# Optimization experiments

Measured on AMD Instinct MI355X. Metric: run time of the kernel, lower is better.

The kernel has to match this reference:

```python
import jax, jax.numpy as jnp
import numpy as np

B = 128        # graphs in batch
GW = 30        # grid width (nodes per graph = GW*GW)
IW = 90        # image width = 3*GW for k=7,s=3,p=2 conv transpose
C_IN = 32
HID = [64, 64, 32]
R = 8          # num relations
NB = 4         # num bases
N = B * GW * GW          # 115200 nodes
E = N * 8                # 921600 edges
NEG_SLOPE = 0.01         # F.leaky_relu default


def setup_inputs() -> dict:
    key = jax.random.key(0)
    ks = jax.random.split(key, 24)
    inp = {
        "features": jax.random.normal(ks[0], (N, C_IN), jnp.float32),
        "src": jax.random.randint(ks[1], (E,), 0, N),
        "dst": jax.random.randint(ks[2], (E,), 0, N),
        "etypes": jax.random.randint(ks[3], (E,), 0, R),
        "norm": jax.random.uniform(ks[4], (E,), jnp.float32),
    }
    dims = [C_IN] + HID
    for l in range(3):
        din, dout = dims[l], dims[l + 1]
        s = 1.0 / np.sqrt(din)
        inp[f"bases{l}"] = jax.random.normal(ks[5 + 4 * l], (NB, din, dout), jnp.float32) * s
        inp[f"comp{l}"] = jax.random.normal(ks[6 + 4 * l], (R, NB), jnp.float32) * (1.0 / np.sqrt(NB))
        inp[f"loop{l}"] = jax.random.normal(ks[7 + 4 * l], (din, dout), jnp.float32) * s
        inp[f"bias{l}"] = jnp.zeros((dout,), jnp.float32)
    inp["conv_w"] = jax.random.normal(ks[20], (HID[-1], 1, 7, 7), jnp.float32) * 0.05  # torch ConvT layout (Cin,Cout,kH,kW)
    inp["conv_b"] = jnp.zeros((1,), jnp.float32)
    return inp


def _rel_graph_conv(h, bases, comp, loop_w, bias, src, dst, etypes, norm, act):
    # basis decomposition: W_r = sum_b comp[r,b] * bases[b]   -> (R, in, out)
    W = jnp.einsum("rb,bio->rio", comp, bases)
    # project every node by every relation weight, then gather per edge
    proj = jnp.einsum("ni,rio->nro", h, W)          # (N, R, out)
    msg = proj[src, etypes] * norm[:, None]          # (E, out)
    agg = jax.ops.segment_sum(msg, dst, num_segments=h.shape[0])
    out = agg + h @ loop_w + bias                    # self-loop + bias (DGL defaults)
    return act(out)


def _conv_transpose(x, w_torch, b, stride, pad):
    # torch ConvTranspose2d(w: (Cin,Cout,kH,kW)) == dilated conv with flipped kernel
    k = w_torch.shape[-1]
    w = jnp.flip(w_torch, (2, 3)).transpose(1, 0, 2, 3)  # -> OIHW
    p = k - 1 - pad
    y = jax.lax.conv_general_dilated(
        x, w, window_strides=(1, 1), padding=[(p, p), (p, p)],
        lhs_dilation=(stride, stride),
        dimension_numbers=("NCHW", "OIHW", "NCHW"))
    return y + b[None, :, None, None]


def reference(features, src, dst, etypes, norm,
              bases0, comp0, loop0, bias0,
              bases1, comp1, loop1, bias1,
              bases2, comp2, loop2, bias2,
              conv_w, conv_b):
    leaky = lambda x: jnp.where(x >= 0, x, NEG_SLOPE * x)
    h = _rel_graph_conv(features, bases0, comp0, loop0, bias0, src, dst, etypes, norm, leaky)
    h = _rel_graph_conv(h, bases1, comp1, loop1, bias1, src, dst, etypes, norm, leaky)
    logits = _rel_graph_conv(h, bases2, comp2, loop2, bias2, src, dst, etypes, norm, jax.nn.sigmoid)
    # every graph has exactly GW*GW nodes -> vectorized decode (replaces per-graph loop)
    x = logits.reshape(B, GW, GW, HID[-1]).transpose(0, 3, 1, 2)  # (B, C, GW, GW)
    y = jax.nn.sigmoid(_conv_transpose(x, conv_w, conv_b, stride=3, pad=2))  # (B,1,IW,IW)
    return y.reshape(B, IW, IW)
```

## Files before the change

kernel.cpp:

```cpp
#include <hip/hip_runtime.h>
#include <hip/hip_bf16.h>

#define B_GR   128
#define GWID   30
#define IWID   90
#define C_IN   32
#define R_REL  8
#define NBAS   4
#define N_NODES (B_GR*GWID*GWID)
#define E_EDGES (N_NODES*8)
#define NEG_SLOPE 0.01f

#define SCAN_BLOCKS (N_NODES/256)

typedef __attribute__((ext_vector_type(8))) __bf16 bf16x8;
typedef __attribute__((ext_vector_type(4))) float f32x4;

__global__ void k_bases_t(const float* __restrict__ bases, __bf16* __restrict__ Bt,
                          int din, int dout) {
    int idx = blockIdx.x*256 + threadIdx.x;
    int tot = NBAS*din*dout;
    if (idx >= tot) return;
    int b = idx/(dout*din), rem = idx%(dout*din);
    int c = rem/din, k = rem%din;
    Bt[idx] = (__bf16)bases[((size_t)b*din + k)*dout + c];
}
__global__ void k_loop_t(const float* __restrict__ loopw, __bf16* __restrict__ loopt,
                         int din, int dout) {
    int idx = blockIdx.x*256 + threadIdx.x;
    if (idx >= din*dout) return;
    int c = idx/din, k = idx%din;
    loopt[idx] = (__bf16)loopw[(size_t)k*dout + c];
}

__global__ void k_deg(const int* __restrict__ dst, int* __restrict__ deg) {
    int e = blockIdx.x*256 + threadIdx.x;
    if (e < E_EDGES) atomicAdd(&deg[dst[e]], 1);
}
__global__ __launch_bounds__(256) void k_scan1(const int* __restrict__ deg,
                                               int* __restrict__ rowptr,
                                               int* __restrict__ bsum) {
    __shared__ int s[256], s2[256];
    const int tid = threadIdx.x, gid = blockIdx.x*256 + tid;
    int v = deg[gid];
    s[tid] = v;
    __syncthreads();
    int* cur = s; int* nxt = s2;
    for (int d = 1; d < 256; d <<= 1) {
        int val = cur[tid];
        if (tid >= d) val += cur[tid - d];
        nxt[tid] = val;
        __syncthreads();
        int* t = cur; cur = nxt; nxt = t;
    }
    rowptr[gid] = cur[tid] - v;
    if (tid == 255) bsum[blockIdx.x] = cur[255];
}
__global__ __launch_bounds__(512) void k_scan2(int* __restrict__ bsum, int* __restrict__ rowptr) {
    __shared__ int s[512], s2[512];
    const int tid = threadIdx.x;
    int v = (tid < SCAN_BLOCKS) ? bsum[tid] : 0;
    s[tid] = v;
    __syncthreads();
    int* cur = s; int* nxt = s2;
    for (int d = 1; d < 512; d <<= 1) {
        int val = cur[tid];
        if (tid >= d) val += cur[tid - d];
        nxt[tid] = val;
        __syncthreads();
        int* t = cur; cur = nxt; nxt = t;
    }
    if (tid < SCAN_BLOCKS) bsum[tid] = cur[tid] - v;
    if (tid == 0) rowptr[N_NODES] = E_EDGES;
}
__global__ void k_scan3(int* __restrict__ rowptr, const int* __restrict__ bsum,
                        int* __restrict__ cursor) {
    int gid = blockIdx.x*256 + threadIdx.x;
    int v = rowptr[gid] + bsum[blockIdx.x];
    rowptr[gid] = v;
    cursor[gid] = v;
}
__global__ void k_scatter_pack(const int* __restrict__ src, const int* __restrict__ dst,
                               const int* __restrict__ et, const float* __restrict__ norm,
                               int* __restrict__ cursor, int2* __restrict__ pmeta) {
    int e = blockIdx.x*256 + threadIdx.x;
    if (e < E_EDGES) {
        int pos = atomicAdd(&cursor[dst[e]], 1);
        int2 m;
        m.x = src[e] | (et[e] << 24);
        m.y = __float_as_int(norm[e]);
        pmeta[pos] = m;
    }
}

template<int DIN, int DOUT, int ACT, int IN_F32, int OUT_F32, int MINW>
__global__ __launch_bounds__(256, MINW) void k_fusedb(
        const void* __restrict__ hin, const __bf16* __restrict__ Bt,
        const __bf16* __restrict__ loopt, const float* __restrict__ bias,
        const float* __restrict__ comp, const int* __restrict__ rowptr,
        const int2* __restrict__ pmeta, void* __restrict__ hout) {
    constexpr int KS = DIN/32;
    constexpr int NF = DOUT/16;
    const int tid = threadIdx.x;
    const int w = tid >> 6, l = tid & 63;
    const int m = l & 15, g = l >> 4;
    const int nb = blockIdx.x*64 + w*16;
    const int node = nb + m;

    f32x4 acc[NF];
    #pragma unroll
    for (int nf = 0; nf < NF; ++nf) acc[nf] = (f32x4){0.f,0.f,0.f,0.f};

    float ka[NBAS][KS][8];
    #pragma unroll
    for (int b = 0; b < NBAS; ++b)
        #pragma unroll
        for (int ks = 0; ks < KS; ++ks)
            #pragma unroll
            for (int c = 0; c < 8; ++c) ka[b][ks][c] = 0.f;

    const int jb = rowptr[node], je = rowptr[node+1];
    int2 mt = pmeta[jb];
    for (int j = jb; j < je; ++j) {
        const int2 mtn = pmeta[j+1];
        const int p = mt.x & 0xFFFFFF;
        const int et = ((unsigned)mt.x) >> 24;
        const float nm = __int_as_float(mt.y);
        const float4 cw = *(const float4*)(comp + et*NBAS);
        const float w0 = nm*cw.x, w1 = nm*cw.y, w2 = nm*cw.z, w3 = nm*cw.w;
        float hv[KS][8];
        if (IN_F32) {
            const float* hp = (const float*)hin + (size_t)p*DIN + g*8;
            #pragma unroll
            for (int ks = 0; ks < KS; ++ks) {
                float4 v0 = *(const float4*)(hp + ks*32);
                float4 v1 = *(const float4*)(hp + ks*32 + 4);
                hv[ks][0]=v0.x; hv[ks][1]=v0.y; hv[ks][2]=v0.z; hv[ks][3]=v0.w;
                hv[ks][4]=v1.x; hv[ks][5]=v1.y; hv[ks][6]=v1.z; hv[ks][7]=v1.w;
            }
        } else {
            const __bf16* hp = (const __bf16*)hin + (size_t)p*DIN + g*8;
            #pragma unroll
            for (int ks = 0; ks < KS; ++ks) {
                bf16x8 v = *(const bf16x8*)(hp + ks*32);
                #pragma unroll
                for (int c = 0; c < 8; ++c) hv[ks][c] = (float)v[c];
            }
        }
        #pragma unroll
        for (int ks = 0; ks < KS; ++ks) {
            #pragma unroll
            for (int c = 0; c < 8; ++c) {
                ka[0][ks][c] += w0*hv[ks][c];
                ka[1][ks][c] += w1*hv[ks][c];
                ka[2][ks][c] += w2*hv[ks][c];
                ka[3][ks][c] += w3*hv[ks][c];
            }
        }
        mt = mtn;
    }

    #pragma unroll
    for (int b = 0; b < NBAS; ++b) {
        #pragma unroll
        for (int ks = 0; ks < KS; ++ks) {
            bf16x8 fa;
            #pragma unroll
            for (int c = 0; c < 8; ++c) fa[c] = (__bf16)ka[b][ks][c];
            #pragma unroll
            for (int nf = 0; nf < NF; ++nf) {
                bf16x8 fb = *(const bf16x8*)(Bt + ((size_t)b*DOUT + nf*16 + m)*DIN
                                             + ks*32 + g*8);
                acc[nf] = __builtin_amdgcn_mfma_f32_16x16x32_bf16(fa, fb, acc[nf], 0, 0, 0);
            }
        }
    }

    #pragma unroll
    for (int ks = 0; ks < KS; ++ks) {
        bf16x8 fa;
        if (IN_F32) {
            const float* hp = (const float*)hin + (size_t)node*DIN + ks*32 + g*8;
            float4 v0 = *(const float4*)hp;
            float4 v1 = *(const float4*)(hp + 4);
            fa[0]=(__bf16)v0.x; fa[1]=(__bf16)v0.y; fa[2]=(__bf16)v0.z; fa[3]=(__bf16)v0.w;
            fa[4]=(__bf16)v1.x; fa[5]=(__bf16)v1.y; fa[6]=(__bf16)v1.z; fa[7]=(__bf16)v1.w;
        } else {
            fa = *(const bf16x8*)((const __bf16*)hin + (size_t)node*DIN + ks*32 + g*8);
        }
        #pragma unroll
        for (int nf = 0; nf < NF; ++nf) {
            bf16x8 fb = *(const bf16x8*)(loopt + (size_t)(nf*16 + m)*DIN + ks*32 + g*8);
            acc[nf] = __builtin_amdgcn_mfma_f32_16x16x32_bf16(fa, fb, acc[nf], 0, 0, 0);
        }
    }

    #pragma unroll
    for (int nf = 0; nf < NF; ++nf) {
        const int col = nf*16 + m;
        const float bv = bias[col];
        #pragma unroll
        for (int ri = 0; ri < 4; ++ri) {
            const int orow = nb + g*4 + ri;
            float v = acc[nf][ri] + bv;
            if (ACT == 0) v = (v >= 0.f) ? v : NEG_SLOPE*v;
            else          v = 1.f/(1.f + __expf(-v));
            if (OUT_F32) ((float*)hout)[(size_t)orow*DOUT + col] = v;
            else         ((__bf16*)hout)[(size_t)orow*DOUT + col] = (__bf16)v;
        }
    }
}

__global__ __launch_bounds__(256) void k_convt_f32(const float* __restrict__ logits,
        const float* __restrict__ w, const float* __restrict__ cb, float* __restrict__ out) {
    __shared__ float s_w[49*32];
    const int tid = threadIdx.x;
    for (int idx = tid; idx < 49*32; idx += 256) {
        int tap = idx/32, c = idx%32;
        s_w[tap*32 + c] = w[c*49 + tap];
    }
    __syncthreads();
    int gidx = blockIdx.x*256 + tid;
    if (gidx >= B_GR*IWID*IWID) return;
    int b = gidx/(IWID*IWID);
    int rem = gidx%(IWID*IWID);
    int oy = rem/IWID, ox = rem%IWID;

    const int py = (oy+2)%3, qy = (oy+2)/3;
    const int px = (ox+2)%3, qx = (ox+2)/3;

    float acc = cb[0];
    #pragma unroll
    for (int sy = 0; sy < 3; ++sy) {
        const int ky = py + 3*sy;
        const int iy = qy - sy;
        if (ky > 6 || iy < 0 || iy >= GWID) continue;
        #pragma unroll
        for (int sx = 0; sx < 3; ++sx) {
            const int kx = px + 3*sx;
            const int ix = qx - sx;
            if (kx > 6 || ix < 0 || ix >= GWID) continue;
            const float4* xp = (const float4*)&logits[(((size_t)b*GWID + iy)*GWID + ix)*32];
            const float4* wp = (const float4*)&s_w[(ky*7 + kx)*32];
            #pragma unroll
            for (int c4 = 0; c4 < 8; ++c4) {
                float4 xv = xp[c4], wv = wp[c4];
                acc += xv.x*wv.x + xv.y*wv.y + xv.z*wv.z + xv.w*wv.w;
            }
        }
    }
    out[gidx] = 1.f/(1.f + __expf(-acc));
}

extern "C" void kernel_launch(void* const* d_in, const int* in_sizes, int n_in,
                              void* d_out, int out_size, void* d_ws, size_t ws_size,
                              hipStream_t stream) {
    const float* features = (const float*)d_in[0];
    const int*   src      = (const int*)  d_in[1];
    const int*   dst      = (const int*)  d_in[2];
    const int*   etypes   = (const int*)  d_in[3];
    const float* norm     = (const float*)d_in[4];
    const float* bases0 = (const float*)d_in[5];
    const float* comp0  = (const float*)d_in[6];
    const float* loop0  = (const float*)d_in[7];
    const float* bias0  = (const float*)d_in[8];
    const float* bases1 = (const float*)d_in[9];
    const float* comp1  = (const float*)d_in[10];
    const float* loop1  = (const float*)d_in[11];
    const float* bias1  = (const float*)d_in[12];
    const float* bases2 = (const float*)d_in[13];
    const float* comp2  = (const float*)d_in[14];
    const float* loop2  = (const float*)d_in[15];
    const float* bias2  = (const float*)d_in[16];
    const float* conv_w = (const float*)d_in[17];
    const float* conv_b = (const float*)d_in[18];
    float* out = (float*)d_out;

    const int ebl = (E_EDGES + 255)/256;
    float* ws = (float*)d_ws;
    auto pad4 = [](size_t v){ return (v + 3) & ~(size_t)3; };

    size_t off = 0;
    __bf16* Bt0   = (__bf16*)(ws + off); off += (size_t)NBAS*32*64/2;
    __bf16* Bt1   = (__bf16*)(ws + off); off += (size_t)NBAS*64*64/2;
    __bf16* Bt2   = (__bf16*)(ws + off); off += (size_t)NBAS*64*32/2;
    __bf16* lt0   = (__bf16*)(ws + off); off += (size_t)64*32/2;
    __bf16* lt1   = (__bf16*)(ws + off); off += (size_t)64*64/2;
    __bf16* lt2   = (__bf16*)(ws + off); off += (size_t)32*64/2;
    __bf16* h1    = (__bf16*)(ws + off); off += (size_t)N_NODES*64/2;
    __bf16* h2    = (__bf16*)(ws + off); off += (size_t)N_NODES*64/2;
    float*  lg    = (float*)(ws + off);  off += (size_t)N_NODES*32;
    int* rowptr   = (int*)(ws + off); off += pad4((size_t)N_NODES + 4);
    int* deg      = (int*)(ws + off); off += (size_t)N_NODES;
    int* bsum     = (int*)(ws + off); off += 512;
    int2* pmeta   = (int2*)(ws + off); off += (size_t)(E_EDGES + 4)*2;

    k_bases_t<<<(NBAS*32*64 + 255)/256, 256, 0, stream>>>(bases0, Bt0, 32, 64);
    k_bases_t<<<(NBAS*64*64 + 255)/256, 256, 0, stream>>>(bases1, Bt1, 64, 64);
    k_bases_t<<<(NBAS*64*32 + 255)/256, 256, 0, stream>>>(bases2, Bt2, 64, 32);
    k_loop_t<<<(32*64 + 255)/256, 256, 0, stream>>>(loop0, lt0, 32, 64);
    k_loop_t<<<(64*64 + 255)/256, 256, 0, stream>>>(loop1, lt1, 64, 64);
    k_loop_t<<<(64*32 + 255)/256, 256, 0, stream>>>(loop2, lt2, 64, 32);

    hipMemsetAsync(deg, 0, (size_t)N_NODES*sizeof(int), stream);
    k_deg  <<<ebl, 256, 0, stream>>>(dst, deg);
    k_scan1<<<SCAN_BLOCKS, 256, 0, stream>>>(deg, rowptr, bsum);
    k_scan2<<<1, 512, 0, stream>>>(bsum, rowptr);
    k_scan3<<<SCAN_BLOCKS, 256, 0, stream>>>(rowptr, bsum, deg);
    k_scatter_pack<<<ebl, 256, 0, stream>>>(src, dst, etypes, norm, deg, pmeta);

    const int NROWT = N_NODES/64;

    k_fusedb<32,64,0,1,0,4><<<NROWT, 256, 0, stream>>>(features, Bt0, lt0, bias0, comp0,
                                                       rowptr, pmeta, h1);
    k_fusedb<64,64,0,0,0,3><<<NROWT, 256, 0, stream>>>(h1, Bt1, lt1, bias1, comp1,
                                                       rowptr, pmeta, h2);
    k_fusedb<64,32,1,0,1,3><<<NROWT, 256, 0, stream>>>(h2, Bt2, lt2, bias2, comp2,
                                                       rowptr, pmeta, lg);

    k_convt_f32<<<(B_GR*IWID*IWID + 255)/256, 256, 0, stream>>>(lg, conv_w, conv_b, out);
}
```

Before: 337.9 us.

## Split each node's edge list across four waves and reduce partial results in LDS

Each block now covers 16 nodes instead of 64. The four waves each take a quarter of every node's incoming edges, aggregate them, and run their own basis MFMAs. Waves 1-3 write their accumulators to shared memory, and wave 0 adds them, applies the self-loop, bias and activation, then stores. This shortens the serial per-lane gather loop and adds memory-level parallelism. The cost is four times the basis MFMA work and weight loads, plus an LDS reduction and a barrier, with three waves idle during the epilogue.

```diff
diff --git a/kernel.cpp b/kernel.cpp
--- a/kernel.cpp
+++ b/kernel.cpp
@@ -94,23 +94,30 @@
 }
 
 template<int DIN, int DOUT, int ACT, int IN_F32, int OUT_F32, int MINW>
-__global__ __launch_bounds__(256, MINW) void k_fusedb(
+__global__ __launch_bounds__(256, MINW) void k_fusedb4(
         const void* __restrict__ hin, const __bf16* __restrict__ Bt,
         const __bf16* __restrict__ loopt, const float* __restrict__ bias,
         const float* __restrict__ comp, const int* __restrict__ rowptr,
         const int2* __restrict__ pmeta, void* __restrict__ hout) {
     constexpr int KS = DIN/32;
     constexpr int NF = DOUT/16;
+    __shared__ float lds_acc[3][NF*4][64];
     const int tid = threadIdx.x;
     const int w = tid >> 6, l = tid & 63;
     const int m = l & 15, g = l >> 4;
-    const int nb = blockIdx.x*64 + w*16;
-    const int node = nb + m;
+    const int node0 = blockIdx.x*16;
+    const int node = node0 + m;
 
     f32x4 acc[NF];
     #pragma unroll
     for (int nf = 0; nf < NF; ++nf) acc[nf] = (f32x4){0.f,0.f,0.f,0.f};
 
+    const int jb = rowptr[node], je = rowptr[node+1];
+    const int len = je - jb;
+    const int q = (len + 3) >> 2;
+    const int wb = jb + w*q;
+    const int we = (wb + q < je) ? (wb + q) : je;
+
     float ka[NBAS][KS][8];
     #pragma unroll
     for (int b = 0; b < NBAS; ++b)
@@ -119,45 +126,46 @@
             #pragma unroll
             for (int c = 0; c < 8; ++c) ka[b][ks][c] = 0.f;
 
-    const int jb = rowptr[node], je = rowptr[node+1];
-    int2 mt = pmeta[jb];
-    for (int j = jb; j < je; ++j) {
-        const int2 mtn = pmeta[j+1];
-        const int p = mt.x & 0xFFFFFF;
-        const int et = ((unsigned)mt.x) >> 24;
-        const float nm = __int_as_float(mt.y);
-        const float4 cw = *(const float4*)(comp + et*NBAS);
-        const float w0 = nm*cw.x, w1 = nm*cw.y, w2 = nm*cw.z, w3 = nm*cw.w;
-        float hv[KS][8];
-        if (IN_F32) {
-            const float* hp = (const float*)hin + (size_t)p*DIN + g*8;
+    if (wb < we) {
+        int2 mt = pmeta[wb];
+        for (int j = wb; j < we; ++j) {
+            const int2 mtn = pmeta[j+1];
+            const int p = mt.x & 0xFFFFFF;
+            const int et = ((unsigned)mt.x) >> 24;
+            const float nm = __int_as_float(mt.y);
+            const float4 cw = *(const float4*)(comp + et*NBAS);
+            const float w0 = nm*cw.x, w1 = nm*cw.y, w2 = nm*cw.z, w3 = nm*cw.w;
+            float hv[KS][8];
+            if (IN_F32) {
+                const float* hp = (const float*)hin + (size_t)p*DIN + g*8;
+                #pragma unroll
+                for (int ks = 0; ks < KS; ++ks) {
+                    float4 v0 = *(const float4*)(hp + ks*32);
+                    float4 v1 = *(const float4*)(hp + ks*32 + 4);
+                    hv[ks][0]=v0.x; hv[ks][1]=v0.y; hv[ks][2]=v0.z; hv[ks][3]=v0.w;
+                    hv[ks][4]=v1.x; hv[ks][5]=v1.y; hv[ks][6]=v1.z; hv[ks][7]=v1.w;
+                }
+            } else {
+                const __bf16* hp = (const __bf16*)hin + (size_t)p*DIN + g*8;
+                #pragma unroll
+                for (int ks = 0; ks < KS; ++ks) {
+                    bf16x8 v = *(const bf16x8*)(hp + ks*32);
+                    #pragma unroll
+                    for (int c = 0; c < 8; ++c) hv[ks][c] = (float)v[c];
+                }
+            }
             #pragma unroll
             for (int ks = 0; ks < KS; ++ks) {
-                float4 v0 = *(const float4*)(hp + ks*32);
-                float4 v1 = *(const float4*)(hp + ks*32 + 4);
-                hv[ks][0]=v0.x; hv[ks][1]=v0.y; hv[ks][2]=v0.z; hv[ks][3]=v0.w;
-                hv[ks][4]=v1.x; hv[ks][5]=v1.y; hv[ks][6]=v1.z; hv[ks][7]=v1.w;
-            }
-        } else {
-            const __bf16* hp = (const __bf16*)hin + (size_t)p*DIN + g*8;
-            #pragma unroll
-            for (int ks = 0; ks < KS; ++ks) {
-                bf16x8 v = *(const bf16x8*)(hp + ks*32);
                 #pragma unroll
-                for (int c = 0; c < 8; ++c) hv[ks][c] = (float)v[c];
-            }
-        }
-        #pragma unroll
-        for (int ks = 0; ks < KS; ++ks) {
-            #pragma unroll
-            for (int c = 0; c < 8; ++c) {
-                ka[0][ks][c] += w0*hv[ks][c];
-                ka[1][ks][c] += w1*hv[ks][c];
-                ka[2][ks][c] += w2*hv[ks][c];
-                ka[3][ks][c] += w3*hv[ks][c];
-            }
-        }
-        mt = mtn;
+                for (int c = 0; c < 8; ++c) {
+                    ka[0][ks][c] += w0*hv[ks][c];
+                    ka[1][ks][c] += w1*hv[ks][c];
+                    ka[2][ks][c] += w2*hv[ks][c];
+                    ka[3][ks][c] += w3*hv[ks][c];
+                }
+            }
+            mt = mtn;
+        }
     }
 
     #pragma unroll
@@ -176,37 +184,52 @@
         }
     }
 
-    #pragma unroll
-    for (int ks = 0; ks < KS; ++ks) {
-        bf16x8 fa;
-        if (IN_F32) {
-            const float* hp = (const float*)hin + (size_t)node*DIN + ks*32 + g*8;
-            float4 v0 = *(const float4*)hp;
-            float4 v1 = *(const float4*)(hp + 4);
-            fa[0]=(__bf16)v0.x; fa[1]=(__bf16)v0.y; fa[2]=(__bf16)v0.z; fa[3]=(__bf16)v0.w;
-            fa[4]=(__bf16)v1.x; fa[5]=(__bf16)v1.y; fa[6]=(__bf16)v1.z; fa[7]=(__bf16)v1.w;
-        } else {
-            fa = *(const bf16x8*)((const __bf16*)hin + (size_t)node*DIN + ks*32 + g*8);
-        }
+    if (w == 0) {
+        #pragma unroll
+        for (int ks = 0; ks < KS; ++ks) {
+            bf16x8 fa;
+            if (IN_F32) {
+                const float* hp = (const float*)hin + (size_t)node*DIN + ks*32 + g*8;
+                float4 v0 = *(const float4*)hp;
+                float4 v1 = *(const float4*)(hp + 4);
+                fa[0]=(__bf16)v0.x; fa[1]=(__bf16)v0.y; fa[2]=(__bf16)v0.z; fa[3]=(__bf16)v0.w;
+                fa[4]=(__bf16)v1.x; fa[5]=(__bf16)v1.y; fa[6]=(__bf16)v1.z; fa[7]=(__bf16)v1.w;
+            } else {
+                fa = *(const bf16x8*)((const __bf16*)hin + (size_t)node*DIN + ks*32 + g*8);
+            }
+            #pragma unroll
+            for (int nf = 0; nf < NF; ++nf) {
+                bf16x8 fb = *(const bf16x8*)(loopt + (size_t)(nf*16 + m)*DIN + ks*32 + g*8);
+                acc[nf] = __builtin_amdgcn_mfma_f32_16x16x32_bf16(fa, fb, acc[nf], 0, 0, 0);
+            }
+        }
+    } else {
+        #pragma unroll
+        for (int nf = 0; nf < NF; ++nf)
+            #pragma unroll
+            for (int ri = 0; ri < 4; ++ri)
+                lds_acc[w-1][nf*4 + ri][l] = acc[nf][ri];
+    }
+    __syncthreads();
+
+    if (w == 0) {
         #pragma unroll
         for (int nf = 0; nf < NF; ++nf) {
-            bf16x8 fb = *(const bf16x8*)(loopt + (size_t)(nf*16 + m)*DIN + ks*32 + g*8);
-            acc[nf] = __builtin_amdgcn_mfma_f32_16x16x32_bf16(fa, fb, acc[nf], 0, 0, 0);
-        }
-    }
-
-    #pragma unroll
-    for (int nf = 0; nf < NF; ++nf) {
-        const int col = nf*16 + m;
-        const float bv = bias[col];
-        #pragma unroll
-        for (int ri = 0; ri < 4; ++ri) {
-            const int orow = nb + g*4 + ri;
-            float v = acc[nf][ri] + bv;
-            if (ACT == 0) v = (v >= 0.f) ? v : NEG_SLOPE*v;
-            else          v = 1.f/(1.f + __expf(-v));
-            if (OUT_F32) ((float*)hout)[(size_t)orow*DOUT + col] = v;
-            else         ((__bf16*)hout)[(size_t)orow*DOUT + col] = (__bf16)v;
+            const int col = nf*16 + m;
+            const float bv = bias[col];
+            #pragma unroll
+            for (int ri = 0; ri < 4; ++ri) {
+                float v = acc[nf][ri]
+                        + lds_acc[0][nf*4 + ri][l]
+                        + lds_acc[1][nf*4 + ri][l]
+                        + lds_acc[2][nf*4 + ri][l]
+                        + bv;
+                if (ACT == 0) v = (v >= 0.f) ? v : NEG_SLOPE*v;
+                else          v = 1.f/(1.f + __expf(-v));
+                const int orow = node0 + g*4 + ri;
+                if (OUT_F32) ((float*)hout)[(size_t)orow*DOUT + col] = v;
+                else         ((__bf16*)hout)[(size_t)orow*DOUT + col] = (__bf16)v;
+            }
         }
     }
 }
@@ -293,7 +316,7 @@
     int* rowptr   = (int*)(ws + off); off += pad4((size_t)N_NODES + 4);
     int* deg      = (int*)(ws + off); off += (size_t)N_NODES;
     int* bsum     = (int*)(ws + off); off += 512;
-    int2* pmeta   = (int2*)(ws + off); off += (size_t)(E_EDGES + 4)*2;
+    int2* pmeta   = (int2*)(ws + off); off += (size_t)(E_EDGES + 8)*2;
 
     k_bases_t<<<(NBAS*32*64 + 255)/256, 256, 0, stream>>>(bases0, Bt0, 32, 64);
     k_bases_t<<<(NBAS*64*64 + 255)/256, 256, 0, stream>>>(bases1, Bt1, 64, 64);
@@ -309,14 +332,14 @@
     k_scan3<<<SCAN_BLOCKS, 256, 0, stream>>>(rowptr, bsum, deg);
     k_scatter_pack<<<ebl, 256, 0, stream>>>(src, dst, etypes, norm, deg, pmeta);
 
-    const int NROWT = N_NODES/64;
-
-    k_fusedb<32,64,0,1,0,4><<<NROWT, 256, 0, stream>>>(features, Bt0, lt0, bias0, comp0,
-                                                       rowptr, pmeta, h1);
-    k_fusedb<64,64,0,0,0,3><<<NROWT, 256, 0, stream>>>(h1, Bt1, lt1, bias1, comp1,
-                                                       rowptr, pmeta, h2);
-    k_fusedb<64,32,1,0,1,3><<<NROWT, 256, 0, stream>>>(h2, Bt2, lt2, bias2, comp2,
-                                                       rowptr, pmeta, lg);
+    const int NBL = N_NODES/16;
+
+    k_fusedb4<32,64,0,1,0,4><<<NBL, 256, 0, stream>>>(features, Bt0, lt0, bias0, comp0,
+                                                      rowptr, pmeta, h1);
+    k_fusedb4<64,64,0,0,0,3><<<NBL, 256, 0, stream>>>(h1, Bt1, lt1, bias1, comp1,
+                                                      rowptr, pmeta, h2);
+    k_fusedb4<64,32,1,0,1,3><<<NBL, 256, 0, stream>>>(h2, Bt2, lt2, bias2, comp2,
+                                                      rowptr, pmeta, lg);
 
     k_convt_f32<<<(B_GR*IWID*IWID + 255)/256, 256, 0, stream>>>(lg, conv_w, conv_b, out);
 }
```

Result: slower. 451.3 us (+33.5%).

## Sort nodes by in-degree so wavefronts process equal-length edge lists

Applied to the files above, without the earlier changes.

Adds a degree histogram, a prefix scan and a scatter that build a permutation of nodes ordered by in-degree. The three fused graph-conv kernels then map each lane to perm[...] and write outputs through that permutation. The aim is to cut divergence in the per-node edge loop, where lanes in a wavefront otherwise wait for the longest neighbour list. The cost is three extra small kernels with global atomics on 64 counters, plus scattered loads and stores of node rows that were contiguous before.

```diff
diff --git a/kernel.cpp b/kernel.cpp
--- a/kernel.cpp
+++ b/kernel.cpp
@@ -12,6 +12,7 @@
 #define NEG_SLOPE 0.01f
 
 #define SCAN_BLOCKS (N_NODES/256)
+#define DBUCK 64
 
 typedef __attribute__((ext_vector_type(8))) __bf16 bf16x8;
 typedef __attribute__((ext_vector_type(4))) float f32x4;
@@ -93,19 +94,41 @@
     }
 }
 
+__global__ void k_hist_deg(const int* __restrict__ rowptr, int* __restrict__ dhist) {
+    int n = blockIdx.x*256 + threadIdx.x;
+    if (n >= N_NODES) return;
+    int d = rowptr[n+1] - rowptr[n];
+    atomicAdd(&dhist[d < DBUCK ? d : DBUCK-1], 1);
+}
+__global__ void k_scan64(const int* __restrict__ dhist, int* __restrict__ dcur) {
+    if (threadIdx.x == 0 && blockIdx.x == 0) {
+        int acc = 0;
+        for (int i = 0; i < DBUCK; ++i) { dcur[i] = acc; acc += dhist[i]; }
+    }
+}
+__global__ void k_scatter_perm(const int* __restrict__ rowptr, int* __restrict__ dcur,
+                               int* __restrict__ perm) {
+    int n = blockIdx.x*256 + threadIdx.x;
+    if (n >= N_NODES) return;
+    int d = rowptr[n+1] - rowptr[n];
+    int pos = atomicAdd(&dcur[d < DBUCK ? d : DBUCK-1], 1);
+    perm[pos] = n;
+}
+
 template<int DIN, int DOUT, int ACT, int IN_F32, int OUT_F32, int MINW>
 __global__ __launch_bounds__(256, MINW) void k_fusedb(
         const void* __restrict__ hin, const __bf16* __restrict__ Bt,
         const __bf16* __restrict__ loopt, const float* __restrict__ bias,
         const float* __restrict__ comp, const int* __restrict__ rowptr,
-        const int2* __restrict__ pmeta, void* __restrict__ hout) {
+        const int2* __restrict__ pmeta, const int* __restrict__ perm,
+        void* __restrict__ hout) {
     constexpr int KS = DIN/32;
     constexpr int NF = DOUT/16;
     const int tid = threadIdx.x;
     const int w = tid >> 6, l = tid & 63;
     const int m = l & 15, g = l >> 4;
     const int nb = blockIdx.x*64 + w*16;
-    const int node = nb + m;
+    const int node = perm[nb + m];
 
     f32x4 acc[NF];
     #pragma unroll
@@ -195,18 +218,20 @@
         }
     }
 
+    int orow[4];
+    #pragma unroll
+    for (int ri = 0; ri < 4; ++ri) orow[ri] = perm[nb + g*4 + ri];
     #pragma unroll
     for (int nf = 0; nf < NF; ++nf) {
         const int col = nf*16 + m;
         const float bv = bias[col];
         #pragma unroll
         for (int ri = 0; ri < 4; ++ri) {
-            const int orow = nb + g*4 + ri;
             float v = acc[nf][ri] + bv;
             if (ACT == 0) v = (v >= 0.f) ? v : NEG_SLOPE*v;
             else          v = 1.f/(1.f + __expf(-v));
-            if (OUT_F32) ((float*)hout)[(size_t)orow*DOUT + col] = v;
-            else         ((__bf16*)hout)[(size_t)orow*DOUT + col] = (__bf16)v;
+            if (OUT_F32) ((float*)hout)[(size_t)orow[ri]*DOUT + col] = v;
+            else         ((__bf16*)hout)[(size_t)orow[ri]*DOUT + col] = (__bf16)v;
         }
     }
 }
@@ -293,7 +318,11 @@
     int* rowptr   = (int*)(ws + off); off += pad4((size_t)N_NODES + 4);
     int* deg      = (int*)(ws + off); off += (size_t)N_NODES;
     int* bsum     = (int*)(ws + off); off += 512;
-    int2* pmeta   = (int2*)(ws + off); off += (size_t)(E_EDGES + 4)*2;
+    int* perm     = (int*)(ws + off); off += (size_t)N_NODES;
+    int* dhist    = (int*)(ws + off); off += DBUCK;
+    int* dcur     = (int*)(ws + off); off += DBUCK;
+    off = pad4(off);
+    int2* pmeta   = (int2*)(ws + off); off += (size_t)(E_EDGES + 8)*2;
 
     k_bases_t<<<(NBAS*32*64 + 255)/256, 256, 0, stream>>>(bases0, Bt0, 32, 64);
     k_bases_t<<<(NBAS*64*64 + 255)/256, 256, 0, stream>>>(bases1, Bt1, 64, 64);
@@ -309,14 +338,19 @@
     k_scan3<<<SCAN_BLOCKS, 256, 0, stream>>>(rowptr, bsum, deg);
     k_scatter_pack<<<ebl, 256, 0, stream>>>(src, dst, etypes, norm, deg, pmeta);
 
+    hipMemsetAsync(dhist, 0, DBUCK*sizeof(int), stream);
+    k_hist_deg   <<<SCAN_BLOCKS, 256, 0, stream>>>(rowptr, dhist);
+    k_scan64     <<<1, 64, 0, stream>>>(dhist, dcur);
+    k_scatter_perm<<<SCAN_BLOCKS, 256, 0, stream>>>(rowptr, dcur, perm);
+
     const int NROWT = N_NODES/64;
 
     k_fusedb<32,64,0,1,0,4><<<NROWT, 256, 0, stream>>>(features, Bt0, lt0, bias0, comp0,
-                                                       rowptr, pmeta, h1);
+                                                       rowptr, pmeta, perm, h1);
     k_fusedb<64,64,0,0,0,3><<<NROWT, 256, 0, stream>>>(h1, Bt1, lt1, bias1, comp1,
-                                                       rowptr, pmeta, h2);
+                                                       rowptr, pmeta, perm, h2);
     k_fusedb<64,32,1,0,1,3><<<NROWT, 256, 0, stream>>>(h2, Bt2, lt2, bias2, comp2,
-                                                       rowptr, pmeta, lg);
+                                                       rowptr, pmeta, perm, lg);
 
     k_convt_f32<<<(B_GR*IWID*IWID + 255)/256, 256, 0, stream>>>(lg, conv_w, conv_b, out);
 }
```

Measured after the change: 1.138 ms. 3.37x slower.

## Split K dimension across wave pairs in 64-input RGCN layers

Applied to the files above, without the earlier changes.

Adds a kernel for the two 64-input layers in which each pair of waves shares 16 nodes and each wave handles half of the input channels. The per-node basis accumulators drop from 4x16 to 4x8 floats per lane, which lowers register pressure and allows a higher waves-per-EU bound. Partial MFMA results are reduced through LDS before bias and activation. The cost is twice as many threads walking each edge list, redundant metadata loads, and an extra block-wide barrier.

```diff
diff --git a/kernel.cpp b/kernel.cpp
--- a/kernel.cpp
+++ b/kernel.cpp
@@ -207,6 +207,101 @@
             else          v = 1.f/(1.f + __expf(-v));
             if (OUT_F32) ((float*)hout)[(size_t)orow*DOUT + col] = v;
             else         ((__bf16*)hout)[(size_t)orow*DOUT + col] = (__bf16)v;
+        }
+    }
+}
+
+template<int DOUT, int ACT, int OUT_F32, int MINW>
+__global__ __launch_bounds__(256, MINW) void k_fusedb_ks(
+        const __bf16* __restrict__ hin, const __bf16* __restrict__ Bt,
+        const __bf16* __restrict__ loopt, const float* __restrict__ bias,
+        const float* __restrict__ comp, const int* __restrict__ rowptr,
+        const int2* __restrict__ pmeta, void* __restrict__ hout) {
+    constexpr int DIN = 64;
+    constexpr int NF = DOUT/16;
+    __shared__ float lds_acc[2][NF*4][64];
+    const int tid = threadIdx.x;
+    const int w = tid >> 6, l = tid & 63;
+    const int pair = w >> 1, kh = w & 1;
+    const int m = l & 15, g = l >> 4;
+    const int nb = blockIdx.x*32 + pair*16;
+    const int node = nb + m;
+    const int kcol = kh*32 + g*8;
+
+    f32x4 acc[NF];
+    #pragma unroll
+    for (int nf = 0; nf < NF; ++nf) acc[nf] = (f32x4){0.f,0.f,0.f,0.f};
+
+    float ka[NBAS][8];
+    #pragma unroll
+    for (int b = 0; b < NBAS; ++b)
+        #pragma unroll
+        for (int c = 0; c < 8; ++c) ka[b][c] = 0.f;
+
+    const int jb = rowptr[node], je = rowptr[node+1];
+    int2 mt = pmeta[jb];
+    for (int j = jb; j < je; ++j) {
+        const int2 mtn = pmeta[j+1];
+        const int p = mt.x & 0xFFFFFF;
+        const int et = ((unsigned)mt.x) >> 24;
+        const float nm = __int_as_float(mt.y);
+        const float4 cw = *(const float4*)(comp + et*NBAS);
+        const float w0 = nm*cw.x, w1 = nm*cw.y, w2 = nm*cw.z, w3 = nm*cw.w;
+        bf16x8 v = *(const bf16x8*)(hin + (size_t)p*DIN + kcol);
+        #pragma unroll
+        for (int c = 0; c < 8; ++c) {
+            const float hv = (float)v[c];
+            ka[0][c] += w0*hv;
+            ka[1][c] += w1*hv;
+            ka[2][c] += w2*hv;
+            ka[3][c] += w3*hv;
+        }
+        mt = mtn;
+    }
+
+    #pragma unroll
+    for (int b = 0; b < NBAS; ++b) {
+        bf16x8 fa;
+        #pragma unroll
+        for (int c = 0; c < 8; ++c) fa[c] = (__bf16)ka[b][c];
+        #pragma unroll
+        for (int nf = 0; nf < NF; ++nf) {
+            bf16x8 fb = *(const bf16x8*)(Bt + ((size_t)b*DOUT + nf*16 + m)*DIN + kcol);
+            acc[nf] = __builtin_amdgcn_mfma_f32_16x16x32_bf16(fa, fb, acc[nf], 0, 0, 0);
+        }
+    }
+    {
+        bf16x8 fa = *(const bf16x8*)(hin + (size_t)node*DIN + kcol);
+        #pragma unroll
+        for (int nf = 0; nf < NF; ++nf) {
+            bf16x8 fb = *(const bf16x8*)(loopt + (size_t)(nf*16 + m)*DIN + kcol);
+            acc[nf] = __builtin_amdgcn_mfma_f32_16x16x32_bf16(fa, fb, acc[nf], 0, 0, 0);
+        }
+    }
+
+    if (kh == 1) {
+        #pragma unroll
+        for (int nf = 0; nf < NF; ++nf)
+            #pragma unroll
+            for (int ri = 0; ri < 4; ++ri)
+                lds_acc[pair][nf*4 + ri][l] = acc[nf][ri];
+    }
+    __syncthreads();
+
+    if (kh == 0) {
+        #pragma unroll
+        for (int nf = 0; nf < NF; ++nf) {
+            const int col = nf*16 + m;
+            const float bv = bias[col];
+            #pragma unroll
+            for (int ri = 0; ri < 4; ++ri) {
+                float v = acc[nf][ri] + lds_acc[pair][nf*4 + ri][l] + bv;
+                if (ACT == 0) v = (v >= 0.f) ? v : NEG_SLOPE*v;
+                else          v = 1.f/(1.f + __expf(-v));
+                const int orow = nb + g*4 + ri;
+                if (OUT_F32) ((float*)hout)[(size_t)orow*DOUT + col] = v;
+                else         ((__bf16*)hout)[(size_t)orow*DOUT + col] = (__bf16)v;
+            }
         }
     }
 }
@@ -293,7 +388,7 @@
     int* rowptr   = (int*)(ws + off); off += pad4((size_t)N_NODES + 4);
     int* deg      = (int*)(ws + off); off += (size_t)N_NODES;
     int* bsum     = (int*)(ws + off); off += 512;
-    int2* pmeta   = (int2*)(ws + off); off += (size_t)(E_EDGES + 4)*2;
+    int2* pmeta   = (int2*)(ws + off); off += (size_t)(E_EDGES + 8)*2;
 
     k_bases_t<<<(NBAS*32*64 + 255)/256, 256, 0, stream>>>(bases0, Bt0, 32, 64);
     k_bases_t<<<(NBAS*64*64 + 255)/256, 256, 0, stream>>>(bases1, Bt1, 64, 64);
@@ -310,13 +405,14 @@
     k_scatter_pack<<<ebl, 256, 0, stream>>>(src, dst, etypes, norm, deg, pmeta);
 
     const int NROWT = N_NODES/64;
+    const int NSPL  = N_NODES/32;
 
     k_fusedb<32,64,0,1,0,4><<<NROWT, 256, 0, stream>>>(features, Bt0, lt0, bias0, comp0,
                                                        rowptr, pmeta, h1);
-    k_fusedb<64,64,0,0,0,3><<<NROWT, 256, 0, stream>>>(h1, Bt1, lt1, bias1, comp1,
-                                                       rowptr, pmeta, h2);
-    k_fusedb<64,32,1,0,1,3><<<NROWT, 256, 0, stream>>>(h2, Bt2, lt2, bias2, comp2,
-                                                       rowptr, pmeta, lg);
+    k_fusedb_ks<64,0,0,5><<<NSPL, 256, 0, stream>>>(h1, Bt1, lt1, bias1, comp1,
+                                                    rowptr, pmeta, h2);
+    k_fusedb_ks<32,1,1,5><<<NSPL, 256, 0, stream>>>(h2, Bt2, lt2, bias2, comp2,
+                                                    rowptr, pmeta, lg);
 
     k_convt_f32<<<(B_GR*IWID*IWID + 255)/256, 256, 0, stream>>>(lg, conv_w, conv_b, out);
 }
```

Result: slower. 353.4 us (+4.6%).
